# Optimization experiments

Hardware: AMD Instinct MI355X
Metric: run time of the kernel (lower is better)

## Reference

```python
import jax, jax.numpy as jnp
import numpy as np

B, S, D = 8, 4096, 1024
N_LEVELS = 8
L = 8
EPS = 1e-3        # FSQ eps (bound shrink)
LN_EPS = 1e-5     # torch LayerNorm default eps


def setup_inputs() -> dict:
    key = jax.random.key(0)
    k1, k2 = jax.random.split(key)
    regrs = jax.random.normal(k1, (B, S, D), dtype=jnp.float32)
    ln_w = jnp.ones((D,), dtype=jnp.float32)
    ln_b = jnp.zeros((D,), dtype=jnp.float32)
    # nn.Linear(d_model, n_levels, bias=False): weight shape [n_levels, d_model]
    W = jax.random.normal(k2, (N_LEVELS, D), dtype=jnp.float32) * (1.0 / np.sqrt(D))
    return {"regrs": regrs, "ln_w": ln_w, "ln_b": ln_b, "W": W}


def reference(regrs, ln_w, ln_b, W):
    # LayerNorm over last dim (biased variance, matching torch)
    mean = jnp.mean(regrs, axis=-1, keepdims=True)
    var = jnp.mean(jnp.square(regrs - mean), axis=-1, keepdims=True)
    x = (regrs - mean) * jax.lax.rsqrt(var + LN_EPS) * ln_w + ln_b
    # skinny projection to n_levels channels
    z = jnp.einsum('bsd,nd->bsn', x, W)  # [B,S,N_LEVELS]
    half_l = L * (1.0 - EPS) / 2.0
    bounded = half_l * jnp.tanh(z)
    # round with straight-through estimator
    code = bounded + jax.lax.stop_gradient(jnp.round(bounded) - bounded)
    return code
```

## Files before the change

kernel.cpp:

```cpp
#include <hip/hip_runtime.h>
#include <math.h>

#define NLEV 8
#define D_DIM 1024

struct TB  { float  t[8]; };
struct TBD { double t[8]; };

template<int CTRL>
__device__ __forceinline__ float ror_add(float v) {
    int r = __builtin_amdgcn_update_dpp(0, __float_as_int(v), CTRL, 0xF, 0xF, true);
    return v + __int_as_float(r);
}
__device__ __forceinline__ float red16(float v) {
    v = ror_add<0x121>(v);
    v = ror_add<0x122>(v);
    v = ror_add<0x124>(v);
    v = ror_add<0x128>(v);
    return v;
}
__device__ __forceinline__ float wave_allreduce(float v) {
    v = red16(v);
    v += __shfl_xor(v, 16, 64);
    v += __shfl_xor(v, 32, 64);
    return v;
}

__global__ __launch_bounds__(512) void fsq_main(
        const float* __restrict__ xg,
        const float* __restrict__ gg,
        const float* __restrict__ bg,
        const float* __restrict__ Wg,
        float* __restrict__ outg,
        unsigned int* __restrict__ wl,
        int wl_cap, int nrows, TB tb)
{
    __shared__ float Vs[NLEV][D_DIM];
    __shared__ float redc1[8][NLEV];
    __shared__ float redc0[8][NLEV];

    const int tid  = (int)threadIdx.x;
    const int lane = tid & 63;
    const int wv   = tid >> 6;

    {
        const int col = tid * 2;
        const float2 g2 = *(const float2*)(gg + col);
        const float2 b2 = *(const float2*)(bg + col);
        float pc1[NLEV], pc0[NLEV];
        #pragma unroll
        for (int n = 0; n < NLEV; ++n) {
            const float2 w2 = *(const float2*)(Wg + n * D_DIM + col);
            float2 v2;
            v2.x = g2.x * w2.x; v2.y = g2.y * w2.y;
            *(float2*)&Vs[n][col] = v2;
            pc1[n] = v2.x + v2.y;
            pc0[n] = b2.x * w2.x + b2.y * w2.y;
        }
        #pragma unroll
        for (int n = 0; n < NLEV; ++n) {
            pc1[n] = wave_allreduce(pc1[n]);
            pc0[n] = wave_allreduce(pc0[n]);
        }
        if (lane == 0) {
            #pragma unroll
            for (int n = 0; n < NLEV; ++n) { redc1[wv][n] = pc1[n]; redc0[wv][n] = pc0[n]; }
        }
    }
    __syncthreads();
    const int nsel = lane & 7;
    float C1sel = 0.f, C0sel = 0.f;
    #pragma unroll
    for (int w = 0; w < 8; ++w) { C1sel += redc1[w][nsel]; C0sel += redc0[w][nsel]; }

    const long wave_row0 = (long)blockIdx.x * 32 + (long)wv * 4;
    const float4* xb = (const float4*)xg;

    for (int p = 0; p < 4; ++p) {
        const long row = wave_row0 + p;
        if (row >= nrows) break;

        const float4* xr = xb + row * (D_DIM / 4);
        float4 xv0 = xr[lane];
        float4 xv1 = xr[64 + lane];
        float4 xv2 = xr[128 + lane];
        float4 xv3 = xr[192 + lane];

        float s = 0.f, sq = 0.f;
        float acc[NLEV];
        #pragma unroll
        for (int n = 0; n < NLEV; ++n) acc[n] = 0.f;

        #pragma unroll
        for (int j = 0; j < 4; ++j) {
            const float4 a = (j == 0) ? xv0 : (j == 1) ? xv1 : (j == 2) ? xv2 : xv3;
            const int vcol = j * 256 + lane * 4;
            s += (a.x + a.y) + (a.z + a.w);
            sq = fmaf(a.x, a.x, sq); sq = fmaf(a.y, a.y, sq);
            sq = fmaf(a.z, a.z, sq); sq = fmaf(a.w, a.w, sq);
            #pragma unroll
            for (int n = 0; n < NLEV; ++n) {
                const float4 v4 = *(const float4*)&Vs[n][vcol];
                acc[n] = fmaf(a.x, v4.x, acc[n]);
                acc[n] = fmaf(a.y, v4.y, acc[n]);
                acc[n] = fmaf(a.z, v4.z, acc[n]);
                acc[n] = fmaf(a.w, v4.w, acc[n]);
            }
        }

        s = red16(s); sq = red16(sq);
        #pragma unroll
        for (int n = 0; n < NLEV; ++n) acc[n] = red16(acc[n]);

        float u0 = (lane & 4) ? acc[4] : acc[0];
        float u1 = (lane & 4) ? acc[5] : acc[1];
        float u2 = (lane & 4) ? acc[6] : acc[2];
        float u3 = (lane & 4) ? acc[7] : acc[3];
        float w0 = (lane & 2) ? u2 : u0;
        float w1 = (lane & 2) ? u3 : u1;
        float Ssel = (lane & 1) ? w1 : w0;

        Ssel += __shfl_xor(Ssel, 16, 64); Ssel += __shfl_xor(Ssel, 32, 64);
        s    += __shfl_xor(s, 16, 64);    s    += __shfl_xor(s, 32, 64);
        sq   += __shfl_xor(sq, 16, 64);   sq   += __shfl_xor(sq, 32, 64);

        bool flag = false;
        if (lane < NLEV) {
            const float mean = s * (1.0f / 1024.0f);
            const float var  = sq * (1.0f / 1024.0f) - mean * mean;
            const float rstd = 1.0f / sqrtf(var + 1e-5f);
            const float z = rstd * (Ssel - mean * C1sel) + C0sel;
            int cnt = 0;
            float mind = 1e30f;
            #pragma unroll
            for (int k = 0; k < 8; ++k) {
                cnt += (z > tb.t[k]) ? 1 : 0;
                mind = fminf(mind, fabsf(z - tb.t[k]));
            }
            outg[row * NLEV + lane] = (float)(cnt - 4);
            flag = (mind < 1.0e-3f);
        }
        const unsigned long long bal = __ballot(flag);
        if (lane == 0 && bal != 0ULL) {
            const unsigned i = atomicAdd(wl, 1u);
            if (i < (unsigned)wl_cap) wl[16 + i] = (unsigned)row;
        }
    }
}

__global__ __launch_bounds__(256) void fsq_fix(
        const float* __restrict__ xg,
        const float* __restrict__ gg,
        const float* __restrict__ bg,
        const float* __restrict__ Wg,
        float* __restrict__ outg,
        const unsigned int* __restrict__ wl,
        int wl_cap, TBD tbd)
{
    const int tid  = (int)threadIdx.x;
    const int lane = tid & 63;
    const int wv   = tid >> 6;
    const unsigned wave   = blockIdx.x * 4 + wv;
    const unsigned nwaves = gridDim.x * 4;

    unsigned cnt = wl[0];
    if (cnt > (unsigned)wl_cap) cnt = (unsigned)wl_cap;
    if (wave >= cnt) return;

    for (unsigned it = wave; it < cnt; it += nwaves) {
        const long row = (long)wl[16 + it];
        const float4* xb4 = (const float4*)(xg + row * D_DIM);

        double s = 0.0, sq = 0.0;
        #pragma unroll
        for (int j = 0; j < 4; ++j) {
            const float4 x4 = xb4[j * 64 + lane];
            const double x0 = (double)x4.x, x1 = (double)x4.y;
            const double x2 = (double)x4.z, x3 = (double)x4.w;
            s += ((x0 + x1) + (x2 + x3));
            sq = fma(x0, x0, sq); sq = fma(x1, x1, sq);
            sq = fma(x2, x2, sq); sq = fma(x3, x3, sq);
        }
        #pragma unroll
        for (int off = 32; off >= 1; off >>= 1) {
            s  += __shfl_xor(s, off, 64);
            sq += __shfl_xor(sq, off, 64);
        }
        const double mean = s * (1.0 / 1024.0);
        const double var  = sq * (1.0 / 1024.0) - mean * mean;
        const double rstd = 1.0 / sqrt(var + 1e-5);

        double acc[NLEV];
        #pragma unroll
        for (int n = 0; n < NLEV; ++n) acc[n] = 0.0;
        #pragma unroll
        for (int j = 0; j < 4; ++j) {
            const int col = j * 256 + lane * 4;
            const float4 x4 = xb4[j * 64 + lane];
            const float4 g4 = *(const float4*)(gg + col);
            const float4 b4 = *(const float4*)(bg + col);
            const double y0 = fma(((double)x4.x - mean) * rstd, (double)g4.x, (double)b4.x);
            const double y1 = fma(((double)x4.y - mean) * rstd, (double)g4.y, (double)b4.y);
            const double y2 = fma(((double)x4.z - mean) * rstd, (double)g4.z, (double)b4.z);
            const double y3 = fma(((double)x4.w - mean) * rstd, (double)g4.w, (double)b4.w);
            #pragma unroll
            for (int n = 0; n < NLEV; ++n) {
                const float4 w4 = *(const float4*)(Wg + n * D_DIM + col);
                acc[n] = fma(y0, (double)w4.x, acc[n]);
                acc[n] = fma(y1, (double)w4.y, acc[n]);
                acc[n] = fma(y2, (double)w4.z, acc[n]);
                acc[n] = fma(y3, (double)w4.w, acc[n]);
            }
        }
        #pragma unroll
        for (int off = 32; off >= 1; off >>= 1) {
            #pragma unroll
            for (int n = 0; n < NLEV; ++n) acc[n] += __shfl_xor(acc[n], off, 64);
        }

        if (lane < NLEV) {
            double a0 = (lane & 4) ? acc[4] : acc[0];
            double a1 = (lane & 4) ? acc[5] : acc[1];
            double a2 = (lane & 4) ? acc[6] : acc[2];
            double a3 = (lane & 4) ? acc[7] : acc[3];
            double b0 = (lane & 2) ? a2 : a0;
            double b1 = (lane & 2) ? a3 : a1;
            const double z = (lane & 1) ? b1 : b0;
            int c = 0;
            #pragma unroll
            for (int k = 0; k < 8; ++k) c += (z > tbd.t[k]) ? 1 : 0;
            outg[row * NLEV + lane] = (float)(c - 4);
        }
    }
}

extern "C" void kernel_launch(void* const* d_in, const int* in_sizes, int n_in,
                              void* d_out, int out_size, void* d_ws, size_t ws_size,
                              hipStream_t stream) {
    (void)n_in; (void)out_size;
    const float* regrs = (const float*)d_in[0];
    const float* ln_w  = (const float*)d_in[1];
    const float* ln_b  = (const float*)d_in[2];
    const float* W     = (const float*)d_in[3];
    float* out = (float*)d_out;

    const int nrows = in_sizes[0] / D_DIM;
    const int nblocks = (nrows + 31) / 32;

    unsigned int* wl = (unsigned int*)d_ws;
    long cap_l = ((long)(ws_size / 4)) - 16;
    if (cap_l < 0) cap_l = 0;
    if (cap_l > nrows) cap_l = nrows;
    const int wl_cap = (int)cap_l;

    TB tb; TBD tbd;
    for (int k = 0; k < 8; ++k) {
        const double y = ((double)k - 3.5) / 3.996;
        tbd.t[k] = atanh(y);
        tb.t[k]  = (float)tbd.t[k];
    }

    hipMemsetAsync(d_ws, 0, 64, stream);
    fsq_main<<<nblocks, 512, 0, stream>>>(regrs, ln_w, ln_b, W, out, wl, wl_cap, nrows, tb);
    fsq_fix<<<128, 256, 0, stream>>>(regrs, ln_w, ln_b, W, out, wl, wl_cap, tbd);
}
```

Before: 218.0 us.

## Fuse near-threshold fp64 fixup into main kernel, drop worklist and memset

Rows whose fast fp32 projection lands near a rounding threshold are now recomputed in double precision inline, inside the main kernel, from the row data already held in registers (xv0..xv3). This removes the workspace memset, the atomic worklist, and the second fix-up kernel launch along with its re-read of flagged rows from global memory. In exchange the main kernel carries a divergent fp64 path that may raise register pressure and lower occupancy, and waves that hit a flagged row stall on slow fp64 work.

```diff
diff --git a/kernel.cpp b/kernel.cpp
--- a/kernel.cpp
+++ b/kernel.cpp
@@ -26,14 +26,13 @@
     return v;
 }
 
-__global__ __launch_bounds__(512) void fsq_main(
+__global__ __launch_bounds__(512) void fsq_fused(
         const float* __restrict__ xg,
         const float* __restrict__ gg,
         const float* __restrict__ bg,
         const float* __restrict__ Wg,
         float* __restrict__ outg,
-        unsigned int* __restrict__ wl,
-        int wl_cap, int nrows, TB tb)
+        int nrows, TB tb, TBD tbd)
 {
     __shared__ float Vs[NLEV][D_DIM];
     __shared__ float redc1[8][NLEV];
@@ -125,111 +124,84 @@
         sq   += __shfl_xor(sq, 16, 64);   sq   += __shfl_xor(sq, 32, 64);
 
         bool flag = false;
+        int  cnt_fast = 0;
         if (lane < NLEV) {
             const float mean = s * (1.0f / 1024.0f);
             const float var  = sq * (1.0f / 1024.0f) - mean * mean;
             const float rstd = 1.0f / sqrtf(var + 1e-5f);
             const float z = rstd * (Ssel - mean * C1sel) + C0sel;
-            int cnt = 0;
             float mind = 1e30f;
             #pragma unroll
             for (int k = 0; k < 8; ++k) {
-                cnt += (z > tb.t[k]) ? 1 : 0;
+                cnt_fast += (z > tb.t[k]) ? 1 : 0;
                 mind = fminf(mind, fabsf(z - tb.t[k]));
             }
-            outg[row * NLEV + lane] = (float)(cnt - 4);
             flag = (mind < 1.0e-3f);
         }
         const unsigned long long bal = __ballot(flag);
-        if (lane == 0 && bal != 0ULL) {
-            const unsigned i = atomicAdd(wl, 1u);
-            if (i < (unsigned)wl_cap) wl[16 + i] = (unsigned)row;
-        }
-    }
-}
-
-__global__ __launch_bounds__(256) void fsq_fix(
-        const float* __restrict__ xg,
-        const float* __restrict__ gg,
-        const float* __restrict__ bg,
-        const float* __restrict__ Wg,
-        float* __restrict__ outg,
-        const unsigned int* __restrict__ wl,
-        int wl_cap, TBD tbd)
-{
-    const int tid  = (int)threadIdx.x;
-    const int lane = tid & 63;
-    const int wv   = tid >> 6;
-    const unsigned wave   = blockIdx.x * 4 + wv;
-    const unsigned nwaves = gridDim.x * 4;
-
-    unsigned cnt = wl[0];
-    if (cnt > (unsigned)wl_cap) cnt = (unsigned)wl_cap;
-    if (wave >= cnt) return;
-
-    for (unsigned it = wave; it < cnt; it += nwaves) {
-        const long row = (long)wl[16 + it];
-        const float4* xb4 = (const float4*)(xg + row * D_DIM);
-
-        double s = 0.0, sq = 0.0;
-        #pragma unroll
-        for (int j = 0; j < 4; ++j) {
-            const float4 x4 = xb4[j * 64 + lane];
-            const double x0 = (double)x4.x, x1 = (double)x4.y;
-            const double x2 = (double)x4.z, x3 = (double)x4.w;
-            s += ((x0 + x1) + (x2 + x3));
-            sq = fma(x0, x0, sq); sq = fma(x1, x1, sq);
-            sq = fma(x2, x2, sq); sq = fma(x3, x3, sq);
-        }
-        #pragma unroll
-        for (int off = 32; off >= 1; off >>= 1) {
-            s  += __shfl_xor(s, off, 64);
-            sq += __shfl_xor(sq, off, 64);
-        }
-        const double mean = s * (1.0 / 1024.0);
-        const double var  = sq * (1.0 / 1024.0) - mean * mean;
-        const double rstd = 1.0 / sqrt(var + 1e-5);
-
-        double acc[NLEV];
-        #pragma unroll
-        for (int n = 0; n < NLEV; ++n) acc[n] = 0.0;
-        #pragma unroll
-        for (int j = 0; j < 4; ++j) {
-            const int col = j * 256 + lane * 4;
-            const float4 x4 = xb4[j * 64 + lane];
-            const float4 g4 = *(const float4*)(gg + col);
-            const float4 b4 = *(const float4*)(bg + col);
-            const double y0 = fma(((double)x4.x - mean) * rstd, (double)g4.x, (double)b4.x);
-            const double y1 = fma(((double)x4.y - mean) * rstd, (double)g4.y, (double)b4.y);
-            const double y2 = fma(((double)x4.z - mean) * rstd, (double)g4.z, (double)b4.z);
-            const double y3 = fma(((double)x4.w - mean) * rstd, (double)g4.w, (double)b4.w);
-            #pragma unroll
-            for (int n = 0; n < NLEV; ++n) {
-                const float4 w4 = *(const float4*)(Wg + n * D_DIM + col);
-                acc[n] = fma(y0, (double)w4.x, acc[n]);
-                acc[n] = fma(y1, (double)w4.y, acc[n]);
-                acc[n] = fma(y2, (double)w4.z, acc[n]);
-                acc[n] = fma(y3, (double)w4.w, acc[n]);
-            }
-        }
-        #pragma unroll
-        for (int off = 32; off >= 1; off >>= 1) {
-            #pragma unroll
-            for (int n = 0; n < NLEV; ++n) acc[n] += __shfl_xor(acc[n], off, 64);
-        }
-
-        if (lane < NLEV) {
-            double a0 = (lane & 4) ? acc[4] : acc[0];
-            double a1 = (lane & 4) ? acc[5] : acc[1];
-            double a2 = (lane & 4) ? acc[6] : acc[2];
-            double a3 = (lane & 4) ? acc[7] : acc[3];
-            double b0 = (lane & 2) ? a2 : a0;
-            double b1 = (lane & 2) ? a3 : a1;
-            const double z = (lane & 1) ? b1 : b0;
-            int c = 0;
-            #pragma unroll
-            for (int k = 0; k < 8; ++k) c += (z > tbd.t[k]) ? 1 : 0;
-            outg[row * NLEV + lane] = (float)(c - 4);
+
+        if (bal == 0ULL) {
+            if (lane < NLEV) outg[row * NLEV + lane] = (float)(cnt_fast - 4);
+        } else {
+            double ds = 0.0, dsq = 0.0;
+            #pragma unroll
+            for (int j = 0; j < 4; ++j) {
+                const float4 a = (j == 0) ? xv0 : (j == 1) ? xv1 : (j == 2) ? xv2 : xv3;
+                const double x0 = (double)a.x, x1 = (double)a.y;
+                const double x2 = (double)a.z, x3 = (double)a.w;
+                ds += ((x0 + x1) + (x2 + x3));
+                dsq = fma(x0, x0, dsq); dsq = fma(x1, x1, dsq);
+                dsq = fma(x2, x2, dsq); dsq = fma(x3, x3, dsq);
+            }
+            #pragma unroll
+            for (int off = 32; off >= 1; off >>= 1) {
+                ds  += __shfl_xor(ds, off, 64);
+                dsq += __shfl_xor(dsq, off, 64);
+            }
+            const double mean = ds * (1.0 / 1024.0);
+            const double var  = dsq * (1.0 / 1024.0) - mean * mean;
+            const double rstd = 1.0 / sqrt(var + 1e-5);
+
+            double dacc[NLEV];
+            #pragma unroll
+            for (int n = 0; n < NLEV; ++n) dacc[n] = 0.0;
+            #pragma unroll
+            for (int j = 0; j < 4; ++j) {
+                const int col = j * 256 + lane * 4;
+                const float4 a = (j == 0) ? xv0 : (j == 1) ? xv1 : (j == 2) ? xv2 : xv3;
+                const float4 g4 = *(const float4*)(gg + col);
+                const float4 b4 = *(const float4*)(bg + col);
+                const double y0 = fma(((double)a.x - mean) * rstd, (double)g4.x, (double)b4.x);
+                const double y1 = fma(((double)a.y - mean) * rstd, (double)g4.y, (double)b4.y);
+                const double y2 = fma(((double)a.z - mean) * rstd, (double)g4.z, (double)b4.z);
+                const double y3 = fma(((double)a.w - mean) * rstd, (double)g4.w, (double)b4.w);
+                #pragma unroll
+                for (int n = 0; n < NLEV; ++n) {
+                    const float4 w4 = *(const float4*)(Wg + n * D_DIM + col);
+                    dacc[n] = fma(y0, (double)w4.x, dacc[n]);
+                    dacc[n] = fma(y1, (double)w4.y, dacc[n]);
+                    dacc[n] = fma(y2, (double)w4.z, dacc[n]);
+                    dacc[n] = fma(y3, (double)w4.w, dacc[n]);
+                }
+            }
+            #pragma unroll
+            for (int off = 32; off >= 1; off >>= 1) {
+                #pragma unroll
+                for (int n = 0; n < NLEV; ++n) dacc[n] += __shfl_xor(dacc[n], off, 64);
+            }
+            if (lane < NLEV) {
+                double a0 = (lane & 4) ? dacc[4] : dacc[0];
+                double a1 = (lane & 4) ? dacc[5] : dacc[1];
+                double a2 = (lane & 4) ? dacc[6] : dacc[2];
+                double a3 = (lane & 4) ? dacc[7] : dacc[3];
+                double b0 = (lane & 2) ? a2 : a0;
+                double b1 = (lane & 2) ? a3 : a1;
+                const double z = (lane & 1) ? b1 : b0;
+                int c = 0;
+                #pragma unroll
+                for (int k = 0; k < 8; ++k) c += (z > tbd.t[k]) ? 1 : 0;
+                outg[row * NLEV + lane] = (float)(c - 4);
+            }
         }
     }
 }
@@ -237,7 +209,7 @@
 extern "C" void kernel_launch(void* const* d_in, const int* in_sizes, int n_in,
                               void* d_out, int out_size, void* d_ws, size_t ws_size,
                               hipStream_t stream) {
-    (void)n_in; (void)out_size;
+    (void)n_in; (void)out_size; (void)d_ws; (void)ws_size;
     const float* regrs = (const float*)d_in[0];
     const float* ln_w  = (const float*)d_in[1];
     const float* ln_b  = (const float*)d_in[2];
@@ -246,12 +218,6 @@
 
     const int nrows = in_sizes[0] / D_DIM;
     const int nblocks = (nrows + 31) / 32;
-
-    unsigned int* wl = (unsigned int*)d_ws;
-    long cap_l = ((long)(ws_size / 4)) - 16;
-    if (cap_l < 0) cap_l = 0;
-    if (cap_l > nrows) cap_l = nrows;
-    const int wl_cap = (int)cap_l;
 
     TB tb; TBD tbd;
     for (int k = 0; k < 8; ++k) {
@@ -260,7 +226,5 @@
         tb.t[k]  = (float)tbd.t[k];
     }
 
-    hipMemsetAsync(d_ws, 0, 64, stream);
-    fsq_main<<<nblocks, 512, 0, stream>>>(regrs, ln_w, ln_b, W, out, wl, wl_cap, nrows, tb);
-    fsq_fix<<<128, 256, 0, stream>>>(regrs, ln_w, ln_b, W, out, wl, wl_cap, tbd);
-}
+    fsq_fused<<<nblocks, 512, 0, stream>>>(regrs, ln_w, ln_b, W, out, nrows, tb, tbd);
+}
```

Result: no change. 215.4 us (-1.2%).
